# Kernel tuning notes

Measured on AMD Instinct MI355X. Metric: run time of the kernel, lower is better.

The kernel has to match this reference:

```python
import jax, jax.numpy as jnp
import numpy as np

NEG = 0.01  # LeakyReLU default slope
EPS = 1e-5  # InstanceNorm eps

def conv(x, w, b=None, pad=0, groups=1):
    y = jax.lax.conv_general_dilated(x, w, (1, 1), [(pad, pad), (pad, pad)],
                                     dimension_numbers=('NCHW', 'OIHW', 'NCHW'),
                                     feature_group_count=groups)
    if b is not None:
        y = y + b[None, :, None, None]
    return y

def inorm(x):
    m = jnp.mean(x, axis=(2, 3), keepdims=True)
    v = jnp.var(x, axis=(2, 3), keepdims=True)
    return (x - m) / jnp.sqrt(v + EPS)

def lrelu(x):
    return jax.nn.leaky_relu(x, NEG)

def maxpool2(x):
    return jax.lax.reduce_window(x, -jnp.inf, jax.lax.max, (1, 1, 2, 2), (1, 1, 2, 2), 'VALID')

def setup_inputs() -> dict:
    key = jax.random.key(0)
    ks = jax.random.split(key, 17)
    C = 64
    def w(k, shape, fan_in):
        return (jax.random.normal(k, shape, jnp.float32) * (1.0 / np.sqrt(fan_in)))
    return {
        'x': jax.random.normal(ks[0], (4, 3, 256, 256), jnp.float32),
        'w_proj': w(ks[1], (C, 3, 3, 3), 27), 'b_proj': jnp.zeros((C,), jnp.float32),
        'w_a1': w(ks[2], (C // 4, C, 1, 1), C), 'w_a2': w(ks[3], (C, C // 4, 1, 1), C // 4),
        'w_ref': w(ks[4], (C, 1, 3, 3), 9), 'b_ref': jnp.zeros((C,), jnp.float32),
        'w_fuse': w(ks[5], (C, C, 1, 1), C), 'b_fuse': jnp.zeros((C,), jnp.float32),
        'w_con': w(ks[6], (2 * C * 4, 1, 3, 3), 9),
        'w_u1': w(ks[7], (C, 2 * C * 4, 1, 1), 2 * C * 4), 'b_u1': jnp.zeros((C,), jnp.float32),
        'w_u2': w(ks[8], (C, C, 3, 3), 9 * C), 'b_u2': jnp.zeros((C,), jnp.float32),
        'w_sc': w(ks[9], (C, 2 * C, 1, 1), 2 * C), 'b_sc': jnp.zeros((C,), jnp.float32),
    }

def reference(x, w_proj, b_proj, w_a1, w_a2, w_ref, b_ref, w_fuse, b_fuse,
              w_con, w_u1, b_u1, w_u2, b_u2, w_sc, b_sc):
    xp = conv(x, w_proj, b_proj, pad=1)
    B, C, H, W = xp.shape
    # --- high branch: pywt wavedec2+waverec2 is perfect reconstruction (identity);
    #     torch code detaches -> stop_gradient on the reconstruction path
    xw = jax.lax.stop_gradient(xp)
    a = jnp.mean(xw, axis=(2, 3), keepdims=True)          # AdaptiveAvgPool2d(1)
    a = lrelu(conv(a, w_a1))
    a = jax.nn.sigmoid(conv(a, w_a2))
    xw = xw * a
    xw = conv(xw, w_ref, b_ref, pad=1, groups=C)          # depthwise refine
    xw = lrelu(inorm(xw))
    # --- low branch: FFT low-pass box filter
    f = jnp.fft.fftshift(jnp.fft.fft2(xp), axes=(-2, -1))
    hl = int(H * 0.3 // 2); wl = int(W * 0.3 // 2)
    hc, wc = H // 2, W // 2
    mask = jnp.zeros((H, W), bool).at[hc - hl:hc + hl, wc - wl:wc + wl].set(True)
    low = jnp.fft.ifft2(jnp.fft.ifftshift(f * mask, axes=(-2, -1))).real
    low = lrelu(inorm(conv(low, w_fuse, b_fuse)))
    # --- hypergraph construct / unwrap
    xc = jnp.concatenate([xw, low], axis=1)               # [B, 2C, H, W]
    h = conv(xc, w_con, pad=1, groups=2 * C)              # [B, 2C*k, H, W]
    u = lrelu(inorm(conv(h, w_u1, b_u1)))
    u = lrelu(inorm(conv(u, w_u2, b_u2, pad=1)))
    feat = u + conv(xc, w_sc, b_sc)
    pooled = maxpool2(feat)
    return feat, pooled
```

## Files before the change

### kernel.cpp

```cpp
#include <hip/hip_runtime.h>
#include <hip/hip_bf16.h>

#define WIDTH 256
#define HW 65536
#define IMG 16777216
#define NIMG 256
#define NSPLIT 16

typedef __attribute__((ext_vector_type(8))) short bf8v;
typedef __attribute__((ext_vector_type(4))) float f4v;

__device__ __forceinline__ float lrelu_f(float v){ return v > 0.f ? v : 0.01f*v; }
__device__ __forceinline__ unsigned short bf16u(float v){
    __hip_bfloat16 h = __float2bfloat16(v);
    return *(unsigned short*)&h;
}

__global__ __launch_bounds__(256) void k_statsf(const float* __restrict__ ps, float* __restrict__ st)
{
    const int img = threadIdx.x;
    const float* p = ps + blockIdx.x * (256 * NSPLIT * 2) + img * (NSPLIT * 2);
    float* o = st + blockIdx.x * 512;
    float S = 0.f, S2 = 0.f;
#pragma unroll
    for (int q = 0; q < NSPLIT; q++) { S += p[q * 2]; S2 += p[q * 2 + 1]; }
    const float m = S / 65536.f;
    const float var = S2 / 65536.f - m * m;
    o[img * 2]     = m;
    o[img * 2 + 1] = rsqrtf(var + 1e-5f);
}

__global__ __launch_bounds__(256) void k_attention(const float* __restrict__ ps0,
    const float* __restrict__ wa1, const float* __restrict__ wa2, float* __restrict__ a2o)
{
    __shared__ float means[256];
    __shared__ float a1s[64];
    const int tid = threadIdx.x;
    {
        const float* p = ps0 + tid * (NSPLIT * 2);
        float S = 0.f;
#pragma unroll
        for (int q = 0; q < NSPLIT; q++) S += p[q * 2];
        means[tid] = S * (1.f / 65536.f);
    }
    __syncthreads();
    if (tid < 64) {
        const int b = tid >> 4, o = tid & 15;
        float s = 0.f;
        for (int c = 0; c < 64; c++) s += wa1[o * 64 + c] * means[b * 64 + c];
        a1s[b * 16 + o] = lrelu_f(s);
    }
    __syncthreads();
    {
        const int b = tid >> 6, c = tid & 63;
        float s = 0.f;
#pragma unroll
        for (int o = 0; o < 16; o++) s += wa2[c * 16 + o] * a1s[b * 16 + o];
        a2o[tid] = 1.f / (1.f + expf(-s));
    }
}

__global__ __launch_bounds__(256, 3) void k_proj(const float* __restrict__ x,
    const float* __restrict__ wt, const float* __restrict__ bias,
    float* __restrict__ out, float* __restrict__ ps0)
{
    __shared__ float wl[3][9][32];
    const int tid = threadIdx.x;
    const int og = tid >> 5, xg = tid & 31;
    const int half = blockIdx.x & 1;
    const int y = (blockIdx.x >> 1) & 255;
    const int b = blockIdx.x >> 9;
    const int o_base = half * 32;
    const int o0l = og * 4;
    const int x0 = xg * 8;
    const int split = y & (NSPLIT - 1);

    for (int idx = tid; idx < 3 * 9 * 32; idx += 256) {
        const int o = idx & 31;
        const int rest = idx >> 5;
        const int pos = rest % 9, cc = rest / 9;
        wl[cc][pos][o] = wt[((o_base + o) * 3 + cc) * 9 + pos];
    }
    __syncthreads();

    float acc[4][8];
#pragma unroll
    for (int i = 0; i < 4; i++)
#pragma unroll
        for (int j = 0; j < 8; j++) acc[i][j] = 0.f;

#pragma unroll 2
    for (int cc = 0; cc < 3; cc++) {
        const float* src = x + ((size_t)b * 3 + cc) * HW;
#pragma unroll
        for (int dy = 0; dy < 3; dy++) {
            const int yy = y + dy - 1;
            float vv[10];
            if (yy >= 0 && yy < 256) {
                const float* r = src + (size_t)yy * WIDTH;
                vv[0] = (x0 > 0) ? r[x0 - 1] : 0.f;
                const float4 m0 = *(const float4*)(r + x0);
                const float4 m1 = *(const float4*)(r + x0 + 4);
                vv[1] = m0.x; vv[2] = m0.y; vv[3] = m0.z; vv[4] = m0.w;
                vv[5] = m1.x; vv[6] = m1.y; vv[7] = m1.z; vv[8] = m1.w;
                vv[9] = (x0 < 248) ? r[x0 + 8] : 0.f;
            } else {
#pragma unroll
                for (int q = 0; q < 10; q++) vv[q] = 0.f;
            }
#pragma unroll
            for (int dx = 0; dx < 3; dx++) {
                const float4 w4 = *(const float4*)&wl[cc][dy * 3 + dx][o0l];
                const float wv[4] = { w4.x, w4.y, w4.z, w4.w };
#pragma unroll
                for (int oi = 0; oi < 4; oi++)
#pragma unroll
                    for (int px = 0; px < 8; px++)
                        acc[oi][px] += wv[oi] * vv[px + dx];
            }
        }
    }
#pragma unroll
    for (int oi = 0; oi < 4; oi++) {
        const int o = o_base + o0l + oi;
        const float bv = bias[o];
        const size_t off = ((size_t)(b * 64 + o)) * HW + (size_t)y * WIDTH + x0;
        float4 r0, r1;
        r0.x = acc[oi][0] + bv; r0.y = acc[oi][1] + bv; r0.z = acc[oi][2] + bv; r0.w = acc[oi][3] + bv;
        r1.x = acc[oi][4] + bv; r1.y = acc[oi][5] + bv; r1.z = acc[oi][6] + bv; r1.w = acc[oi][7] + bv;
        *(float4*)(out + off) = r0;
        *(float4*)(out + off + 4) = r1;
        float s  = r0.x + r0.y + r0.z + r0.w + r1.x + r1.y + r1.z + r1.w;
        float s2 = r0.x*r0.x + r0.y*r0.y + r0.z*r0.z + r0.w*r0.w
                 + r1.x*r1.x + r1.y*r1.y + r1.z*r1.z + r1.w*r1.w;
#pragma unroll
        for (int offt = 16; offt > 0; offt >>= 1) {
            s  += __shfl_down(s, offt, 32);
            s2 += __shfl_down(s2, offt, 32);
        }
        if (xg == 0) {
            float* pp = &ps0[((b * 64 + o) * NSPLIT + split) * 2];
            atomicAdd(pp, s);
            atomicAdd(pp + 1, s2);
        }
    }
}

__global__ __launch_bounds__(256) void k_dw(const float* __restrict__ xp, const float* __restrict__ a2,
    const float* __restrict__ wref, const float* __restrict__ bref, float* __restrict__ out,
    float* __restrict__ ps1)
{
    const int tid = threadIdx.x;
    const int img = blockIdx.x >> 6;
    const int y = ((blockIdx.x & 63) << 2) + (tid >> 6);
    const int x0 = (tid & 63) * 4;
    const int c = img & 63;
    const int split = blockIdx.x & (NSPLIT - 1);
    const float* src = xp + (size_t)img * HW;
    float wv[9];
#pragma unroll
    for (int k = 0; k < 9; k++) wv[k] = wref[c * 9 + k];
    const float scale = a2[img], bb = bref[c];

    float a[4] = {0.f, 0.f, 0.f, 0.f};
#pragma unroll
    for (int dy = 0; dy < 3; dy++) {
        const int yy = y + dy - 1;
        if (yy < 0 || yy > 255) continue;
        const float* r = src + (size_t)yy * WIDTH;
        float vv[6];
        vv[0] = (x0 > 0) ? r[x0 - 1] : 0.f;
        const float4 m = *(const float4*)(r + x0);
        vv[1] = m.x; vv[2] = m.y; vv[3] = m.z; vv[4] = m.w;
        vv[5] = (x0 < 252) ? r[x0 + 4] : 0.f;
#pragma unroll
        for (int dx = 0; dx < 3; dx++)
#pragma unroll
            for (int px = 0; px < 4; px++)
                a[px] += wv[dy * 3 + dx] * vv[px + dx];
    }
    float4 o;
    o.x = bb + scale * a[0]; o.y = bb + scale * a[1];
    o.z = bb + scale * a[2]; o.w = bb + scale * a[3];
    *(float4*)(out + (size_t)img * HW + (size_t)y * WIDTH + x0) = o;

    float s  = o.x + o.y + o.z + o.w;
    float s2 = o.x*o.x + o.y*o.y + o.z*o.z + o.w*o.w;
#pragma unroll
    for (int offt = 32; offt > 0; offt >>= 1) {
        s  += __shfl_down(s, offt, 64);
        s2 += __shfl_down(s2, offt, 64);
    }
    __shared__ float ls[4][2];
    const int wid = tid >> 6, lane = tid & 63;
    if (lane == 0) { ls[wid][0] = s; ls[wid][1] = s2; }
    __syncthreads();
    if (tid == 0) {
        const float S  = ls[0][0] + ls[1][0] + ls[2][0] + ls[3][0];
        const float S2 = ls[0][1] + ls[1][1] + ls[2][1] + ls[3][1];
        float* pp = &ps1[(img * NSPLIT + split) * 2];
        atomicAdd(pp, S);
        atomicAdd(pp + 1, S2);
    }
}

__global__ void k_tables(float* __restrict__ kr2, float* __restrict__ ki2)
{
    const int t = blockIdx.x * 256 + threadIdx.x;
    if (t < 512) {
        const int tm = t & 255;
        const double PI = 3.14159265358979323846;
        const double th = 2.0 * PI * (double)tm / 256.0;
        double sr = 1.0;
        for (int k = 1; k <= 37; k++) sr += 2.0 * cos((double)k * th);
        sr += cos(38.0 * th);
        kr2[t] = (float)(sr / 256.0);
        ki2[t] = (float)(-sin(38.0 * th) / 256.0);
    }
}

__global__ __launch_bounds__(256) void k_kmat(const float* __restrict__ kr2, const float* __restrict__ ki2,
    unsigned short* __restrict__ KBr, unsigned short* __restrict__ KBi)
{
    const int n = blockIdx.x, k = threadIdx.x;
    const int d = (n - k) & 255;
    KBr[n * 256 + k] = bf16u(kr2[d]);
    KBi[n * 256 + k] = bf16u(ki2[d]);
}

__global__ __launch_bounds__(256, 2) void k_mdft1(const float* __restrict__ xp,
    const unsigned short* __restrict__ KBr, const unsigned short* __restrict__ KBi,
    unsigned short* __restrict__ TR, unsigned short* __restrict__ TI)
{
    const int tid = threadIdx.x, lane = tid & 63, wave = tid >> 6;
    const int img = blockIdx.x >> 2;
    const int mb = (blockIdx.x >> 1) & 1, nb = blockIdx.x & 1;
    const int M0 = mb * 128 + (wave >> 1) * 64;
    const int N0 = nb * 128 + (wave & 1) * 64;
    const int lrow = lane & 15, lk = lane >> 4;
    const float* Xb = xp + (size_t)img * HW;

    f4v aR[4][4], aI[4][4];
#pragma unroll
    for (int m = 0; m < 4; m++)
#pragma unroll
        for (int n = 0; n < 4; n++) { aR[m][n] = (f4v){0,0,0,0}; aI[m][n] = (f4v){0,0,0,0}; }

#pragma unroll 1
    for (int k0 = 0; k0 < 256; k0 += 32) {
        bf8v af[4];
#pragma unroll
        for (int m = 0; m < 4; m++) {
            const float* rp = Xb + (size_t)(M0 + m * 16 + lrow) * 256 + k0 + lk * 8;
            const float4 a0 = *(const float4*)rp;
            const float4 a1 = *(const float4*)(rp + 4);
            bf8v t;
            t[0] = (short)bf16u(a0.x); t[1] = (short)bf16u(a0.y);
            t[2] = (short)bf16u(a0.z); t[3] = (short)bf16u(a0.w);
            t[4] = (short)bf16u(a1.x); t[5] = (short)bf16u(a1.y);
            t[6] = (short)bf16u(a1.z); t[7] = (short)bf16u(a1.w);
            af[m] = t;
        }
#pragma unroll
        for (int n = 0; n < 4; n++) {
            const int xcol = N0 + n * 16 + lrow;
            const bf8v br = *(const bf8v*)(KBr + xcol * 256 + k0 + lk * 8);
            const bf8v bi = *(const bf8v*)(KBi + xcol * 256 + k0 + lk * 8);
#pragma unroll
            for (int m = 0; m < 4; m++) {
                aR[m][n] = __builtin_amdgcn_mfma_f32_16x16x32_bf16(af[m], br, aR[m][n], 0, 0, 0);
                aI[m][n] = __builtin_amdgcn_mfma_f32_16x16x32_bf16(af[m], bi, aI[m][n], 0, 0, 0);
            }
        }
    }
#pragma unroll
    for (int n = 0; n < 4; n++) {
        const size_t xoff = (size_t)img * HW + (size_t)(N0 + n * 16 + lrow) * 256;
#pragma unroll
        for (int m = 0; m < 4; m++) {
            const size_t off = xoff + M0 + m * 16 + lk * 4;
            const f4v r = aR[m][n], ii = aI[m][n];
            ushort4 ur, ui;
            ur.x = bf16u(r[0]); ur.y = bf16u(r[1]); ur.z = bf16u(r[2]); ur.w = bf16u(r[3]);
            ui.x = bf16u(ii[0]); ui.y = bf16u(ii[1]); ui.z = bf16u(ii[2]); ui.w = bf16u(ii[3]);
            *(ushort4*)(TR + off) = ur;
            *(ushort4*)(TI + off) = ui;
        }
    }
}

__global__ __launch_bounds__(256, 2) void k_mdft2(const unsigned short* __restrict__ TR,
    const unsigned short* __restrict__ TI, const unsigned short* __restrict__ KBr,
    const unsigned short* __restrict__ KBi, float* __restrict__ low)
{
    const int tid = threadIdx.x, lane = tid & 63, wave = tid >> 6;
    const int img = blockIdx.x >> 2;
    const int mb = (blockIdx.x >> 1) & 1, nb = blockIdx.x & 1;
    const int M0 = mb * 128 + (wave >> 1) * 64;
    const int N0 = nb * 128 + (wave & 1) * 64;
    const int lrow = lane & 15, lk = lane >> 4;
    const unsigned short* TRb = TR + (size_t)img * HW;
    const unsigned short* TIb = TI + (size_t)img * HW;

    f4v aR[4][4], aI[4][4];
#pragma unroll
    for (int m = 0; m < 4; m++)
#pragma unroll
        for (int n = 0; n < 4; n++) { aR[m][n] = (f4v){0,0,0,0}; aI[m][n] = (f4v){0,0,0,0}; }

#pragma unroll 1
    for (int k0 = 0; k0 < 256; k0 += 32) {
        bf8v afR[4], afI[4];
#pragma unroll
        for (int m = 0; m < 4; m++) {
            const int ro = (M0 + m * 16 + lrow) * 256 + k0 + lk * 8;
            afR[m] = *(const bf8v*)(TRb + ro);
            afI[m] = *(const bf8v*)(TIb + ro);
        }
#pragma unroll
        for (int n = 0; n < 4; n++) {
            const int ycol = N0 + n * 16 + lrow;
            const bf8v br = *(const bf8v*)(KBr + ycol * 256 + k0 + lk * 8);
            const bf8v bi = *(const bf8v*)(KBi + ycol * 256 + k0 + lk * 8);
#pragma unroll
            for (int m = 0; m < 4; m++) {
                aR[m][n] = __builtin_amdgcn_mfma_f32_16x16x32_bf16(afR[m], br, aR[m][n], 0, 0, 0);
                aI[m][n] = __builtin_amdgcn_mfma_f32_16x16x32_bf16(afI[m], bi, aI[m][n], 0, 0, 0);
            }
        }
    }
#pragma unroll
    for (int n = 0; n < 4; n++) {
        const size_t yoff = (size_t)img * HW + (size_t)(N0 + n * 16 + lrow) * 256;
#pragma unroll
        for (int m = 0; m < 4; m++) {
            const f4v r = aR[m][n], ii = aI[m][n];
            const float4 v = make_float4(r[0] - ii[0], r[1] - ii[1], r[2] - ii[2], r[3] - ii[3]);
            *(float4*)(low + yoff + M0 + m * 16 + lk * 4) = v;
        }
    }
}

__global__ __launch_bounds__(256) void k_weff_bf(const float* __restrict__ w_u1,
    const float* __restrict__ w_con, unsigned short* __restrict__ wbf)
{
    const int f = blockIdx.x * 256 + threadIdx.x;
    if (f >= 73728) return;
    const int ch = f & 31, oc = (f >> 5) & 63, cp = f >> 11;
    const int pos = cp % 9, cb = cp / 9;
    const int g = cb * 32 + ch;
    float s = 0.f;
#pragma unroll
    for (int j = 0; j < 4; j++) s += w_u1[oc * 512 + g * 4 + j] * w_con[(g * 4 + j) * 9 + pos];
    wbf[f] = bf16u(s);
}

template<int CIN>
__global__ __launch_bounds__(256) void k_wcvt(const float* __restrict__ w, unsigned short* __restrict__ wbf)
{
    const int f = blockIdx.x * 256 + threadIdx.x;
    if (f >= 64 * CIN * 9) return;
    const int ch = f & 31, oc = (f >> 5) & 63, cp = f >> 11;
    const int pos = cp % 9, cb = cp / 9;
    const int c = cb * 32 + ch;
    wbf[f] = bf16u(w[oc * CIN * 9 + c * 9 + pos]);
}

template<int CIN>
__global__ __launch_bounds__(256) void k_wcvt1(const float* __restrict__ w, unsigned short* __restrict__ wbf)
{
    const int f = blockIdx.x * 256 + threadIdx.x;
    if (f >= 64 * CIN) return;
    const int ch = f & 31, oc = (f >> 5) & 63, cb = f >> 11;
    wbf[f] = bf16u(w[oc * CIN + cb * 32 + ch]);
}

template<int CIN>
__global__ __launch_bounds__(256, 4) void k_mconv(
    const float* __restrict__ in0, const float* __restrict__ in1,
    const unsigned short* __restrict__ wbf, const float* __restrict__ bias,
    float* __restrict__ out,
    const float* __restrict__ stA, const float* __restrict__ stB,
    float* __restrict__ psOut)
{
    __shared__ unsigned short Xl[4 * 132 * 32];
    __shared__ float sh_ms[2 * CIN];
    __shared__ float red[4][64][2];
    const int tid = threadIdx.x;
    const int lane = tid & 63;
    const int wave = tid >> 6;
    const int xb = (blockIdx.x & 1) * 128;
    const int y0 = ((blockIdx.x >> 1) & 127) * 2;
    const int b = blockIdx.x >> 8;
    const int row_sel = wave >> 1;
    const int px_half = (wave & 1) * 64;
    const int split = blockIdx.x & (NSPLIT - 1);

    for (int i = tid; i < 4 * 132 * 32 / 2; i += 256) ((unsigned int*)Xl)[i] = 0u;
    for (int j = tid; j < 2 * CIN; j += 256) {
        const int cb_ = j >> 6, jj = j & 63;
        const int c = cb_ * 32 + 2 * (jj >> 2) + ((jj & 3) >> 1);
        const float* st = (CIN == 128 && cb_ >= 2) ? stB : stA;
        sh_ms[j] = st[(b * 64 + (c & 63)) * 2 + (jj & 1)];
    }

    f4v acc[4][4];
#pragma unroll
    for (int i = 0; i < 4; i++)
#pragma unroll
        for (int n = 0; n < 4; n++) acc[i][n] = (f4v){0.f, 0.f, 0.f, 0.f};

    const int lrow = lane & 15;
    const int gsl  = lane >> 4;
    const int wlane = lrow * 32 + gsl * 8;

    __syncthreads();

    constexpr int NC = CIN / 32;
#pragma unroll 1
    for (int cb = 0; cb < NC; cb++) {
        const int c0 = cb * 32;
        const bool second = (CIN == 128 && c0 >= 64);
        const float* src = (second ? in1 : in0) + ((size_t)b * 64 + (c0 & 63)) * HW;
        const float* ms = sh_ms + cb * 64;
        {
            const int r = tid >> 6;
            const int yy = y0 - 1 + r;
            if (yy >= 0 && yy <= 255) {
#pragma unroll 1
                for (int s = tid & 63; s < 130; s += 64) {
                    const int x = xb + s - 1;
                    if (x >= 0 && x <= 255) {
                        const float* rp = src + (size_t)yy * WIDTH + x;
                        const int sbase = r * 8448 + s * 64;
                        const int sw = (s >> 1) & 3;
#pragma unroll 4
                        for (int d = 0; d < 16; d++) {
                            float va = rp[(size_t)(2 * d) * HW];
                            float vb = rp[(size_t)(2 * d + 1) * HW];
                            va = lrelu_f((va - ms[4 * d])     * ms[4 * d + 1]);
                            vb = lrelu_f((vb - ms[4 * d + 2]) * ms[4 * d + 3]);
                            const unsigned int dw = (unsigned int)bf16u(va)
                                                  | ((unsigned int)bf16u(vb) << 16);
                            *(unsigned int*)((char*)Xl + sbase
                                + (((d >> 2) ^ sw) << 4) + ((d & 3) << 2)) = dw;
                        }
                    }
                }
            }
        }
        __syncthreads();
#pragma unroll 1
        for (int pos = 0; pos < 9; pos++) {
            const int dy = pos / 3, dx = pos - dy * 3;
            const unsigned short* wp = wbf + (cb * 9 + pos) * 2048 + wlane;
            const bf8v wf0 = *(const bf8v*)(wp);
            const bf8v wf1 = *(const bf8v*)(wp + 512);
            const bf8v wf2 = *(const bf8v*)(wp + 1024);
            const bf8v wf3 = *(const bf8v*)(wp + 1536);
            const int pxe = px_half + lrow + dx;
            const int row = row_sel + dy;
            const char* abase = (const char*)Xl + row * 8448 + pxe * 64
                              + ((gsl ^ ((pxe >> 1) & 3)) << 4);
#pragma unroll
            for (int i = 0; i < 4; i++) {
                const bf8v af = *(const bf8v*)(abase + i * 1024);
                acc[i][0] = __builtin_amdgcn_mfma_f32_16x16x32_bf16(af, wf0, acc[i][0], 0, 0, 0);
                acc[i][1] = __builtin_amdgcn_mfma_f32_16x16x32_bf16(af, wf1, acc[i][1], 0, 0, 0);
                acc[i][2] = __builtin_amdgcn_mfma_f32_16x16x32_bf16(af, wf2, acc[i][2], 0, 0, 0);
                acc[i][3] = __builtin_amdgcn_mfma_f32_16x16x32_bf16(af, wf3, acc[i][3], 0, 0, 0);
            }
        }
        __syncthreads();
    }
    const int yrow = y0 + row_sel;
    const int lk = gsl;
#pragma unroll
    for (int n = 0; n < 4; n++) {
        const float bv = bias[n * 16 + lrow];
        float* po = out + ((size_t)(b * 64) + n * 16 + lrow) * HW
                  + (size_t)yrow * WIDTH + xb + px_half + lk * 4;
        float s = 0.f, s2 = 0.f;
#pragma unroll
        for (int i = 0; i < 4; i++) {
            const f4v a = acc[i][n];
            float4 v;
            v.x = a[0] + bv; v.y = a[1] + bv; v.z = a[2] + bv; v.w = a[3] + bv;
            s  += v.x + v.y + v.z + v.w;
            s2 += v.x*v.x + v.y*v.y + v.z*v.z + v.w*v.w;
            *(float4*)(po + i * 16) = v;
        }
        s  += __shfl_down(s, 32);  s  += __shfl_down(s, 16);
        s2 += __shfl_down(s2, 32); s2 += __shfl_down(s2, 16);
        if (lk == 0) { red[wave][n * 16 + lrow][0] = s; red[wave][n * 16 + lrow][1] = s2; }
    }
    __syncthreads();
    if (tid < 64) {
        const float S  = red[0][tid][0] + red[1][tid][0] + red[2][tid][0] + red[3][tid][0];
        const float S2 = red[0][tid][1] + red[1][tid][1] + red[2][tid][1] + red[3][tid][1];
        float* pp = &psOut[((b * 64 + tid) * NSPLIT + split) * 2];
        atomicAdd(pp, S);
        atomicAdd(pp + 1, S2);
    }
}

template<int CIN, bool ADD, bool NORMIN, bool STATS>
__global__ __launch_bounds__(256, 3) void k_pconv(
    const float* __restrict__ in0, const float* __restrict__ in1,
    const unsigned short* __restrict__ wbf, const float* __restrict__ bias,
    const float* __restrict__ addsrc, float* __restrict__ out,
    const float* __restrict__ stA, const float* __restrict__ stB,
    const float* __restrict__ stAdd, float* __restrict__ psOut)
{
    __shared__ unsigned short Xl[256 * 32];
    __shared__ float sh_ms[2 * CIN];
    __shared__ float red[4][64][2];
    const int tid = threadIdx.x, lane = tid & 63, wave = tid >> 6;
    const int y = blockIdx.x & 255, b = blockIdx.x >> 8;
    const int split = blockIdx.x & (NSPLIT - 1);
    const int lrow = lane & 15, gsl = lane >> 4;
    const int wpx = wave * 64;
    const int wlane = lrow * 32 + gsl * 8;

    if constexpr (NORMIN) {
        for (int j = tid; j < 2 * CIN; j += 256) {
            const int cb_ = j >> 6, jj = j & 63;
            const int c = cb_ * 32 + 2 * (jj >> 2) + ((jj & 3) >> 1);
            const float* st = (CIN == 128 && cb_ >= 2) ? stB : stA;
            sh_ms[j] = st[(b * 64 + (c & 63)) * 2 + (jj & 1)];
        }
    }

    f4v acc[4][4];
#pragma unroll
    for (int m = 0; m < 4; m++)
#pragma unroll
        for (int n = 0; n < 4; n++) acc[m][n] = (f4v){0.f, 0.f, 0.f, 0.f};

    __syncthreads();

    constexpr int NC = CIN / 32;
#pragma unroll 1
    for (int cb = 0; cb < NC; cb++) {
        const int c0 = cb * 32;
        const bool second = (CIN == 128 && c0 >= 64);
        const float* src = (second ? in1 : in0) + ((size_t)b * 64 + (c0 & 63)) * HW
                         + (size_t)y * WIDTH;
        const float* ms = sh_ms + cb * 64;
        {
            const int px = tid;
            const int sw = (px >> 1) & 3;
#pragma unroll 4
            for (int d = 0; d < 16; d++) {
                float va = src[(size_t)(2 * d) * HW + px];
                float vb = src[(size_t)(2 * d + 1) * HW + px];
                if constexpr (NORMIN) {
                    va = lrelu_f((va - ms[4 * d])     * ms[4 * d + 1]);
                    vb = lrelu_f((vb - ms[4 * d + 2]) * ms[4 * d + 3]);
                }
                const unsigned int dw = (unsigned int)bf16u(va)
                                      | ((unsigned int)bf16u(vb) << 16);
                const int byte = px * 64 + (((d >> 2) ^ sw) << 4) + ((d & 3) << 2);
                *(unsigned int*)((char*)Xl + byte) = dw;
            }
        }
        __syncthreads();
        {
            const unsigned short* wp = wbf + cb * 2048 + wlane;
            const bf8v wf0 = *(const bf8v*)(wp);
            const bf8v wf1 = *(const bf8v*)(wp + 512);
            const bf8v wf2 = *(const bf8v*)(wp + 1024);
            const bf8v wf3 = *(const bf8v*)(wp + 1536);
#pragma unroll
            for (int m = 0; m < 4; m++) {
                const int px = wpx + m * 16 + lrow;
                const char* abase = (const char*)Xl + px * 64
                                  + ((gsl ^ ((px >> 1) & 3)) << 4);
                const bf8v af = *(const bf8v*)abase;
                acc[m][0] = __builtin_amdgcn_mfma_f32_16x16x32_bf16(af, wf0, acc[m][0], 0, 0, 0);
                acc[m][1] = __builtin_amdgcn_mfma_f32_16x16x32_bf16(af, wf1, acc[m][1], 0, 0, 0);
                acc[m][2] = __builtin_amdgcn_mfma_f32_16x16x32_bf16(af, wf2, acc[m][2], 0, 0, 0);
                acc[m][3] = __builtin_amdgcn_mfma_f32_16x16x32_bf16(af, wf3, acc[m][3], 0, 0, 0);
            }
        }
        __syncthreads();
    }
    const int lk = gsl;
#pragma unroll
    for (int n = 0; n < 4; n++) {
        const int oc = n * 16 + lrow;
        const float bv = bias[oc];
        float mm = 0.f, ss = 0.f;
        if constexpr (ADD) { mm = stAdd[(b * 64 + oc) * 2]; ss = stAdd[(b * 64 + oc) * 2 + 1]; }
        const size_t orow = ((size_t)(b * 64 + oc)) * HW + (size_t)y * WIDTH;
        float s = 0.f, s2 = 0.f;
#pragma unroll
        for (int m = 0; m < 4; m++) {
            const int px = wpx + m * 16 + lk * 4;
            const f4v a = acc[m][n];
            float r[4] = { a[0] + bv, a[1] + bv, a[2] + bv, a[3] + bv };
            if constexpr (ADD) {
                const float4 av = *(const float4*)(addsrc + orow + px);
                r[0] += lrelu_f((av.x - mm) * ss);
                r[1] += lrelu_f((av.y - mm) * ss);
                r[2] += lrelu_f((av.z - mm) * ss);
                r[3] += lrelu_f((av.w - mm) * ss);
            }
            *(float4*)(out + orow + px) = make_float4(r[0], r[1], r[2], r[3]);
            if constexpr (STATS) {
                s  += r[0] + r[1] + r[2] + r[3];
                s2 += r[0]*r[0] + r[1]*r[1] + r[2]*r[2] + r[3]*r[3];
            }
        }
        if constexpr (STATS) {
            s  += __shfl_down(s, 32);  s  += __shfl_down(s, 16);
            s2 += __shfl_down(s2, 32); s2 += __shfl_down(s2, 16);
            if (lk == 0) { red[wave][oc][0] = s; red[wave][oc][1] = s2; }
        }
    }
    if constexpr (STATS) {
        __syncthreads();
        if (tid < 64) {
            const float S  = red[0][tid][0] + red[1][tid][0] + red[2][tid][0] + red[3][tid][0];
            const float S2 = red[0][tid][1] + red[1][tid][1] + red[2][tid][1] + red[3][tid][1];
            float* pp = &psOut[((b * 64 + tid) * NSPLIT + split) * 2];
            atomicAdd(pp, S);
            atomicAdd(pp + 1, S2);
        }
    }
}

__global__ __launch_bounds__(256) void k_maxpool(const float* __restrict__ feat, float* __restrict__ out)
{
    const int idx = blockIdx.x * 256 + threadIdx.x;
    const int xo = idx & 127;
    const int yo = (idx >> 7) & 127;
    const int img = idx >> 14;
    const float* p = feat + (size_t)img * HW + (size_t)(yo * 2) * WIDTH + xo * 2;
    out[idx] = fmaxf(fmaxf(p[0], p[1]), fmaxf(p[WIDTH], p[WIDTH + 1]));
}

extern "C" void kernel_launch(void* const* d_in, const int* in_sizes, int n_in,
                              void* d_out, int out_size, void* d_ws, size_t ws_size,
                              hipStream_t stream)
{
    const float* x      = (const float*)d_in[0];
    const float* w_proj = (const float*)d_in[1];
    const float* b_proj = (const float*)d_in[2];
    const float* w_a1   = (const float*)d_in[3];
    const float* w_a2   = (const float*)d_in[4];
    const float* w_ref  = (const float*)d_in[5];
    const float* b_ref  = (const float*)d_in[6];
    const float* w_fuse = (const float*)d_in[7];
    const float* b_fuse = (const float*)d_in[8];
    const float* w_con  = (const float*)d_in[9];
    const float* w_u1   = (const float*)d_in[10];
    const float* b_u1   = (const float*)d_in[11];
    const float* w_u2   = (const float*)d_in[12];
    const float* b_u2   = (const float*)d_in[13];
    const float* w_sc   = (const float*)d_in[14];
    const float* b_sc   = (const float*)d_in[15];

    float* wsf  = (float*)d_ws;
    float* buf0 = wsf;
    float* buf1 = wsf + (size_t)IMG;
    float* buf2 = wsf + (size_t)2 * IMG;
    float* aux  = wsf + (size_t)3 * IMG;
    float* a2b  = aux;
    float* kr2  = aux + 256;
    float* ki2  = aux + 768;
    unsigned short* wbfA = (unsigned short*)(aux + 1280);
    unsigned short* wbfB = wbfA + 73728;
    unsigned short* KBr  = wbfB + 36864;
    unsigned short* KBi  = KBr + 65536;
    unsigned short* wbfF = KBi + 65536;
    unsigned short* wbfS = wbfF + 4096;
    float* ps   = aux + 1280 + 120832 + 6144;
    float* st   = ps + 5 * 256 * NSPLIT * 2;

    float* fout = (float*)d_out;
    float* pout = fout + (size_t)IMG;
    unsigned short* T1R = (unsigned short*)buf2;
    unsigned short* T1I = T1R + (size_t)IMG;

    const int PSSLOT = 256 * NSPLIT * 2;

    hipMemsetAsync(ps, 0, 5 * PSSLOT * sizeof(float), stream);
    k_tables<<<2, 256, 0, stream>>>(kr2, ki2);
    k_kmat<<<256, 256, 0, stream>>>(kr2, ki2, KBr, KBi);
    k_weff_bf<<<288, 256, 0, stream>>>(w_u1, w_con, wbfA);
    k_wcvt<64><<<144, 256, 0, stream>>>(w_u2, wbfB);
    k_wcvt1<64><<<16, 256, 0, stream>>>(w_fuse, wbfF);
    k_wcvt1<128><<<32, 256, 0, stream>>>(w_sc, wbfS);
    k_proj<<<2048, 256, 0, stream>>>(x, w_proj, b_proj, buf0, ps);
    k_attention<<<1, 256, 0, stream>>>(ps, w_a1, w_a2, a2b);
    k_dw<<<16384, 256, 0, stream>>>(buf0, a2b, w_ref, b_ref, buf1, ps + PSSLOT);
    k_mdft1<<<1024, 256, 0, stream>>>(buf0, KBr, KBi, T1R, T1I);
    k_mdft2<<<1024, 256, 0, stream>>>(T1R, T1I, KBr, KBi, fout);
    k_pconv<64, false, false, true><<<1024, 256, 0, stream>>>(
        fout, nullptr, wbfF, b_fuse, nullptr, buf0,
        nullptr, nullptr, nullptr, ps + 2 * PSSLOT);
    k_statsf<<<2, 256, 0, stream>>>(ps + PSSLOT, st + 512);
    k_mconv<128><<<1024, 256, 0, stream>>>(buf1, buf0, wbfA, b_u1, fout,
        st + 512, st + 1024, ps + 3 * PSSLOT);
    k_statsf<<<1, 256, 0, stream>>>(ps + 3 * PSSLOT, st + 1536);
    k_mconv<64><<<1024, 256, 0, stream>>>(fout, nullptr, wbfB, b_u2, buf2,
        st + 1536, st + 1536, ps + 4 * PSSLOT);
    k_statsf<<<1, 256, 0, stream>>>(ps + 4 * PSSLOT, st + 2048);
    k_pconv<128, true, true, false><<<1024, 256, 0, stream>>>(
        buf1, buf0, wbfS, b_sc, buf2, fout,
        st + 512, st + 1024, st + 2048, nullptr);
    k_maxpool<<<16384, 256, 0, stream>>>(fout, pout);
}
```

Measured before the change: 543.6 us.

## Widen 3x3 MFMA conv tile to full image rows with 512-thread blocks

The MFMA 3x3 convolution kernel now processes two full 256-pixel rows per block with 8 waves, instead of two half rows with 4 waves. This removes the duplicated halo columns loaded at the half-row boundary and halves the block count. The staging loop becomes a simple one-pixel-per-thread load, and the reduction now sums over 8 waves. LDS use per block roughly doubles and there are fewer blocks, which can reduce occupancy and the number of distinct split slots used for the stats partial sums.

```diff
diff --git a/kernel.cpp b/kernel.cpp
--- a/kernel.cpp
+++ b/kernel.cpp
@@ -376,28 +376,27 @@
 }
 
 template<int CIN>
-__global__ __launch_bounds__(256, 4) void k_mconv(
+__global__ __launch_bounds__(512, 4) void k_mconv(
     const float* __restrict__ in0, const float* __restrict__ in1,
     const unsigned short* __restrict__ wbf, const float* __restrict__ bias,
     float* __restrict__ out,
     const float* __restrict__ stA, const float* __restrict__ stB,
     float* __restrict__ psOut)
 {
-    __shared__ unsigned short Xl[4 * 132 * 32];
+    __shared__ unsigned short Xl[4 * 260 * 32];
     __shared__ float sh_ms[2 * CIN];
-    __shared__ float red[4][64][2];
+    __shared__ float red[8][64][2];
     const int tid = threadIdx.x;
     const int lane = tid & 63;
     const int wave = tid >> 6;
-    const int xb = (blockIdx.x & 1) * 128;
-    const int y0 = ((blockIdx.x >> 1) & 127) * 2;
-    const int b = blockIdx.x >> 8;
-    const int row_sel = wave >> 1;
-    const int px_half = (wave & 1) * 64;
+    const int b = blockIdx.x >> 7;
+    const int y0 = (blockIdx.x & 127) * 2;
+    const int row_sel = wave & 1;
+    const int px_base = (wave >> 1) * 64;
     const int split = blockIdx.x & (NSPLIT - 1);
 
-    for (int i = tid; i < 4 * 132 * 32 / 2; i += 256) ((unsigned int*)Xl)[i] = 0u;
-    for (int j = tid; j < 2 * CIN; j += 256) {
+    for (int i = tid; i < 4 * 260 * 32 / 2; i += 512) ((unsigned int*)Xl)[i] = 0u;
+    for (int j = tid; j < 2 * CIN; j += 512) {
         const int cb_ = j >> 6, jj = j & 63;
         const int c = cb_ * 32 + 2 * (jj >> 2) + ((jj & 3) >> 1);
         const float* st = (CIN == 128 && cb_ >= 2) ? stB : stA;
@@ -424,28 +423,27 @@
         const float* src = (second ? in1 : in0) + ((size_t)b * 64 + (c0 & 63)) * HW;
         const float* ms = sh_ms + cb * 64;
         {
-            const int r = tid >> 6;
-            const int yy = y0 - 1 + r;
-            if (yy >= 0 && yy <= 255) {
-#pragma unroll 1
-                for (int s = tid & 63; s < 130; s += 64) {
-                    const int x = xb + s - 1;
-                    if (x >= 0 && x <= 255) {
-                        const float* rp = src + (size_t)yy * WIDTH + x;
-                        const int sbase = r * 8448 + s * 64;
-                        const int sw = (s >> 1) & 3;
+            const int px = tid & 255;
+            const int rg = tid >> 8;
+            const int px_idx = px + 1;
+            const int sw = (px_idx >> 1) & 3;
+#pragma unroll
+            for (int r2 = 0; r2 < 2; r2++) {
+                const int r = rg * 2 + r2;
+                const int yy = y0 - 1 + r;
+                if (yy < 0 || yy > 255) continue;
+                const float* rp = src + (size_t)yy * WIDTH + px;
 #pragma unroll 4
-                        for (int d = 0; d < 16; d++) {
-                            float va = rp[(size_t)(2 * d) * HW];
-                            float vb = rp[(size_t)(2 * d + 1) * HW];
-                            va = lrelu_f((va - ms[4 * d])     * ms[4 * d + 1]);
-                            vb = lrelu_f((vb - ms[4 * d + 2]) * ms[4 * d + 3]);
-                            const unsigned int dw = (unsigned int)bf16u(va)
-                                                  | ((unsigned int)bf16u(vb) << 16);
-                            *(unsigned int*)((char*)Xl + sbase
-                                + (((d >> 2) ^ sw) << 4) + ((d & 3) << 2)) = dw;
-                        }
-                    }
+                for (int d = 0; d < 16; d++) {
+                    float va = rp[(size_t)(2 * d) * HW];
+                    float vb = rp[(size_t)(2 * d + 1) * HW];
+                    va = lrelu_f((va - ms[4 * d])     * ms[4 * d + 1]);
+                    vb = lrelu_f((vb - ms[4 * d + 2]) * ms[4 * d + 3]);
+                    const unsigned int dw = (unsigned int)bf16u(va)
+                                          | ((unsigned int)bf16u(vb) << 16);
+                    const int byte = r * 16640 + px_idx * 64
+                                   + (((d >> 2) ^ sw) << 4) + ((d & 3) << 2);
+                    *(unsigned int*)((char*)Xl + byte) = dw;
                 }
             }
         }
@@ -458,9 +456,9 @@
             const bf8v wf1 = *(const bf8v*)(wp + 512);
             const bf8v wf2 = *(const bf8v*)(wp + 1024);
             const bf8v wf3 = *(const bf8v*)(wp + 1536);
-            const int pxe = px_half + lrow + dx;
+            const int pxe = px_base + lrow + 1 + dx - 1;
             const int row = row_sel + dy;
-            const char* abase = (const char*)Xl + row * 8448 + pxe * 64
+            const char* abase = (const char*)Xl + row * 16640 + pxe * 64
                               + ((gsl ^ ((pxe >> 1) & 3)) << 4);
 #pragma unroll
             for (int i = 0; i < 4; i++) {
@@ -479,7 +477,7 @@
     for (int n = 0; n < 4; n++) {
         const float bv = bias[n * 16 + lrow];
         float* po = out + ((size_t)(b * 64) + n * 16 + lrow) * HW
-                  + (size_t)yrow * WIDTH + xb + px_half + lk * 4;
+                  + (size_t)yrow * WIDTH + px_base + lk * 4;
         float s = 0.f, s2 = 0.f;
 #pragma unroll
         for (int i = 0; i < 4; i++) {
@@ -496,8 +494,9 @@
     }
     __syncthreads();
     if (tid < 64) {
-        const float S  = red[0][tid][0] + red[1][tid][0] + red[2][tid][0] + red[3][tid][0];
-        const float S2 = red[0][tid][1] + red[1][tid][1] + red[2][tid][1] + red[3][tid][1];
+        float S = 0.f, S2 = 0.f;
+#pragma unroll
+        for (int w = 0; w < 8; w++) { S += red[w][tid][0]; S2 += red[w][tid][1]; }
         float* pp = &psOut[((b * 64 + tid) * NSPLIT + split) * 2];
         atomicAdd(pp, S);
         atomicAdd(pp + 1, S2);
@@ -701,10 +700,10 @@
         fout, nullptr, wbfF, b_fuse, nullptr, buf0,
         nullptr, nullptr, nullptr, ps + 2 * PSSLOT);
     k_statsf<<<2, 256, 0, stream>>>(ps + PSSLOT, st + 512);
-    k_mconv<128><<<1024, 256, 0, stream>>>(buf1, buf0, wbfA, b_u1, fout,
+    k_mconv<128><<<512, 512, 0, stream>>>(buf1, buf0, wbfA, b_u1, fout,
         st + 512, st + 1024, ps + 3 * PSSLOT);
     k_statsf<<<1, 256, 0, stream>>>(ps + 3 * PSSLOT, st + 1536);
-    k_mconv<64><<<1024, 256, 0, stream>>>(fout, nullptr, wbfB, b_u2, buf2,
+    k_mconv<64><<<512, 512, 0, stream>>>(fout, nullptr, wbfB, b_u2, buf2,
         st + 1536, st + 1536, ps + 4 * PSSLOT);
     k_statsf<<<1, 256, 0, stream>>>(ps + 4 * PSSLOT, st + 2048);
     k_pconv<128, true, true, false><<<1024, 256, 0, stream>>>(
```

New measurement: 500.1 us. 8.0% less time.
